# Kernel optimization log

Hardware: AMD Instinct MI355X
Metric: run time of the kernel (lower is better)

## Reference

```python
import jax, jax.numpy as jnp
import numpy as np


def setup_inputs() -> dict:
    key = jax.random.key(0)
    k1, k2, k3 = jax.random.split(key, 3)
    B, R, Din, D = 4096, 4096, 1024, 1024
    x = jax.random.normal(k1, (B, Din), dtype=jnp.float32)
    refs = jax.random.normal(k2, (R, Din), dtype=jnp.float32)
    W = jax.random.normal(k3, (Din, D), dtype=jnp.float32) * (1.0 / np.sqrt(Din))
    b = jnp.zeros((D,), dtype=jnp.float32)
    return {"x": x, "refs": refs, "W": W, "b": b}


def reference(x, refs, W, b) -> jnp.ndarray:
    # feature extractor (linear stand-in for the CResNet embedding)
    vin = x @ W + b          # (B, D)
    vrefs = refs @ W + b     # (R, D)
    # compute_degradation_metric: mean_r ||vin_b - vref_r||^2
    # = ||vin||^2 + mean_r ||vref_r||^2 - 2 * vin @ mean_r(vref_r)
    # Same math as the naive broadcast-sub-square-sum-mean, GEMM-friendly form.
    sq_in = jnp.sum(vin * vin, axis=1)                 # (B,)
    mean_sq_ref = jnp.mean(jnp.sum(vrefs * vrefs, axis=1))  # scalar
    mean_ref = jnp.mean(vrefs, axis=0)                 # (D,)
    cross = vin @ mean_ref                             # (B,)
    degradation_metric = sq_in + mean_sq_ref - 2.0 * cross
    return degradation_metric
```

## Files before the change

### kernel.cpp

```cpp
#include <hip/hip_runtime.h>
#include <hip/hip_bf16.h>
#include <stdint.h>


typedef __attribute__((ext_vector_type(8))) short short8;
typedef __attribute__((ext_vector_type(4))) float f32x4;

__device__ __forceinline__ short f2bf(float f) {
  uint32_t u = __builtin_bit_cast(uint32_t, f);
  uint32_t r = (u + 0x7fffu + ((u >> 16) & 1u)) >> 16;
  return (short)r;
}

#define WS_WT 0u
#define WS_TC 2097152u
#define WS_RR 2101248u

__global__ __launch_bounds__(256) void k_prep(
    const float* __restrict__ W, short* __restrict__ wt,
    float* __restrict__ tcol, float* __restrict__ refrow, float* __restrict__ out) {
  __shared__ short tile[64][68];
  const int b = blockIdx.x, t = threadIdx.x;
  if (b < 256) {
    const int tk = (b >> 4) * 64, tn = (b & 15) * 64;
    const int kk = t >> 4, nn4 = (t & 15) * 4;
#pragma unroll
    for (int p = 0; p < 4; ++p) {
      int k = kk + p * 16;
      float4 v = *(const float4*)&W[(size_t)(tk + k) * 1024 + tn + nn4];
      tile[nn4 + 0][k] = f2bf(v.x);
      tile[nn4 + 1][k] = f2bf(v.y);
      tile[nn4 + 2][k] = f2bf(v.z);
      tile[nn4 + 3][k] = f2bf(v.w);
    }
    __syncthreads();
    const int nn = t >> 4, kk4 = (t & 15) * 4;
#pragma unroll
    for (int p = 0; p < 4; ++p) {
      int n = nn + p * 16;
      uint32_t lo = (uint16_t)tile[n][kk4 + 0] | ((uint32_t)(uint16_t)tile[n][kk4 + 1] << 16);
      uint32_t hi = (uint16_t)tile[n][kk4 + 2] | ((uint32_t)(uint16_t)tile[n][kk4 + 3] << 16);
      *(uint2*)&wt[(size_t)(tn + n) * 1024 + tk + kk4] = make_uint2(lo, hi);
    }
  } else {
    const int i = (b - 256) * 256 + t;
    const float4 z = make_float4(0.f, 0.f, 0.f, 0.f);
    ((float4*)out)[i] = z;
    ((float4*)refrow)[i] = z;
    if (i < 256) ((float4*)tcol)[i] = z;
  }
}

template <bool IS_X>
__global__ __launch_bounds__(512, 4) void k_gemm(
    const float* __restrict__ Am, const short* __restrict__ Wt,
    const float* __restrict__ bias, float* __restrict__ tcol,
    float* __restrict__ refrow, float* __restrict__ out) {
  __shared__ __align__(16) short As[2][128 * 64];
  __shared__ __align__(16) short Bs[2][128 * 64];
  const int t = threadIdx.x;
  const int w = t >> 6, l = t & 63;

  if (IS_X && blockIdx.x >= 256) {
    __shared__ float sh[8];
    float s = 0.f;
    for (int i = t; i < 4096; i += 512) s += refrow[i];
#pragma unroll
    for (int off = 32; off; off >>= 1) s += __shfl_down(s, off, 64);
    if (l == 0) sh[w] = s;
    __syncthreads();
    if (t == 0) {
      float tot = 0.f;
#pragma unroll
      for (int i = 0; i < 8; ++i) tot += sh[i];
      sh[0] = tot * (1.0f / 4096.0f);
    }
    __syncthreads();
    const float ms = sh[0];
    for (int i = t; i < 4096; i += 512) atomicAdd(&out[i], ms);
    return;
  }

  const int wr = w >> 2, wc = w & 3;
  const int bx = blockIdx.x;
  const int mt = bx & 31;
  const int nt = bx >> 5;
  const int m0 = mt * 128;
  const int n0 = nt * 128;

  const int srow = t >> 3;
  const int sslot = t & 7;
  const int arow = t >> 4;
  const int acol = (t & 15) * 4;
  const int asl = (t & 15) >> 1, ah = t & 1;

  f32x4 acc[4][2] = {};
  float4 areg[4];

  auto stageB = [&](int buf, int kt) {
    const int k0 = kt * 64;
#pragma unroll
    for (int issue = 0; issue < 2; ++issue) {
      const int row = srow + issue * 64;
      const int sg = sslot ^ (row & 7);
      const short* gb = Wt + ((size_t)(n0 + row) * 1024 + k0 + sg * 8);
      char* lb = (char*)&Bs[buf][0] + issue * 8192 + w * 1024;
      __builtin_amdgcn_global_load_lds(
          (const __attribute__((address_space(1))) unsigned int*)gb,
          (__attribute__((address_space(3))) unsigned int*)lb, 16, 0, 0);
    }
  };
  auto loadA = [&](int kt) {
    const int k0 = kt * 64;
#pragma unroll
    for (int i = 0; i < 4; ++i) {
      const int r = arow + i * 32;
      areg[i] = *(const float4*)&Am[(size_t)(m0 + r) * 1024 + k0 + acol];
    }
  };
  auto writeA = [&](int buf) {
#pragma unroll
    for (int i = 0; i < 4; ++i) {
      const int r = arow + i * 32;
      uint32_t lo, hi;
      asm("v_cvt_pk_bf16_f32 %0, %1, %2" : "=v"(lo) : "v"(areg[i].x), "v"(areg[i].y));
      asm("v_cvt_pk_bf16_f32 %0, %1, %2" : "=v"(hi) : "v"(areg[i].z), "v"(areg[i].w));
      char* p = (char*)&As[buf][0] + r * 128 + (((asl ^ (r & 7)) * 16) + ah * 8);
      *(uint2*)p = make_uint2(lo, hi);
    }
  };

  loadA(0);
  stageB(0, 0);
  stageB(1, 1);
  writeA(0);
  loadA(1);

  for (int kt = 0; kt < 16; ++kt) {
    if (kt < 15) asm volatile("s_waitcnt vmcnt(6) lgkmcnt(0)" ::: "memory");
    else         asm volatile("s_waitcnt vmcnt(0) lgkmcnt(0)" ::: "memory");
    __builtin_amdgcn_s_barrier();
    const int cur = kt & 1;
    if (kt + 1 < 16) writeA((kt + 1) & 1);
    if (kt + 2 < 16) loadA(kt + 2);
#pragma unroll
    for (int kk = 0; kk < 2; ++kk) {
      short8 af[4], bfr[2];
#pragma unroll
      for (int i = 0; i < 4; ++i) {
        const int ra = wr * 64 + i * 16 + (l & 15);
        const int s = (l >> 4) + kk * 4;
        af[i] = *(const short8*)&As[cur][ra * 64 + ((s ^ (ra & 7)) * 8)];
      }
#pragma unroll
      for (int j = 0; j < 2; ++j) {
        const int rbw = wc * 32 + j * 16 + (l & 15);
        const int s = (l >> 4) + kk * 4;
        bfr[j] = *(const short8*)&Bs[cur][rbw * 64 + ((s ^ (rbw & 7)) * 8)];
      }
      __builtin_amdgcn_s_setprio(1);
#pragma unroll
      for (int i = 0; i < 4; ++i)
#pragma unroll
        for (int j = 0; j < 2; ++j)
          acc[i][j] = __builtin_amdgcn_mfma_f32_16x16x32_bf16(af[i], bfr[j], acc[i][j], 0, 0, 0);
      __builtin_amdgcn_s_setprio(0);
    }
    __builtin_amdgcn_s_barrier();
    if (kt + 2 < 16) stageB(cur, kt + 2);
  }

  float bv[2];
#pragma unroll
  for (int n2 = 0; n2 < 2; ++n2) bv[n2] = bias[n0 + wc * 32 + n2 * 16 + (l & 15)];

  if (IS_X) {
    float tvv[2];
#pragma unroll
    for (int n2 = 0; n2 < 2; ++n2)
      tvv[n2] = tcol[n0 + wc * 32 + n2 * 16 + (l & 15)] * (1.0f / 4096.0f);
#pragma unroll
    for (int m4 = 0; m4 < 4; ++m4) {
#pragma unroll
      for (int j = 0; j < 4; ++j) {
        float sq = 0.f, cr = 0.f;
#pragma unroll
        for (int n2 = 0; n2 < 2; ++n2) {
          const float v = acc[m4][n2][j] + bv[n2];
          sq += v * v;
          cr += v * tvv[n2];
        }
        float comb = sq - 2.0f * cr;
#pragma unroll
        for (int off = 1; off < 16; off <<= 1) comb += __shfl_xor(comb, off, 64);
        if ((l & 15) == 0) {
          const int rm = m0 + wr * 64 + m4 * 16 + (l >> 4) * 4 + j;
          atomicAdd(&out[rm], comb);
        }
      }
    }
  } else {
#pragma unroll
    for (int m4 = 0; m4 < 4; ++m4) {
#pragma unroll
      for (int j = 0; j < 4; ++j) {
        float sq = 0.f;
#pragma unroll
        for (int n2 = 0; n2 < 2; ++n2) {
          const float v = acc[m4][n2][j] + bv[n2];
          sq += v * v;
        }
#pragma unroll
        for (int off = 1; off < 16; off <<= 1) sq += __shfl_xor(sq, off, 64);
        if ((l & 15) == 0) {
          const int rm = m0 + wr * 64 + m4 * 16 + (l >> 4) * 4 + j;
          atomicAdd(&refrow[rm], sq);
        }
      }
    }
#pragma unroll
    for (int n2 = 0; n2 < 2; ++n2) {
      float cs = 16.0f * bv[n2];
#pragma unroll
      for (int m4 = 0; m4 < 4; ++m4)
#pragma unroll
        for (int j = 0; j < 4; ++j) cs += acc[m4][n2][j];
      cs += __shfl_xor(cs, 16, 64);
      cs += __shfl_xor(cs, 32, 64);
      if ((l >> 4) == 0)
        atomicAdd(&tcol[n0 + wc * 32 + n2 * 16 + (l & 15)], cs);
    }
  }
}

extern "C" void kernel_launch(void* const* d_in, const int* in_sizes, int n_in,
                              void* d_out, int out_size, void* d_ws, size_t ws_size,
                              hipStream_t stream) {
  const float* x    = (const float*)d_in[0];
  const float* refs = (const float*)d_in[1];
  const float* W    = (const float*)d_in[2];
  const float* bias = (const float*)d_in[3];
  float* out = (float*)d_out;
  char* ws = (char*)d_ws;

  short* wt     = (short*)(ws + WS_WT);
  float* tcol   = (float*)(ws + WS_TC);
  float* refrow = (float*)(ws + WS_RR);

  hipLaunchKernelGGL(k_prep, dim3(260), dim3(256), 0, stream, W, wt, tcol, refrow, out);
  hipLaunchKernelGGL(k_gemm<false>, dim3(256), dim3(512), 0, stream,
                     refs, wt, bias, tcol, refrow, out);
  hipLaunchKernelGGL(k_gemm<true>, dim3(257), dim3(512), 0, stream,
                     x, wt, bias, tcol, refrow, out);
}
```

Baseline: 51.54 us.

## Merge ref and x GEMMs into one launch with an atomic-counter dependency

Fuses the two GEMM launches into a single 512-block grid. The first 256 blocks process refs and bump a global counter. The x blocks run their GEMM mainloop, then spin until all ref blocks have finished before applying the mean-ref cross term. The final mean-square reduction moves into block 256. This removes a kernel-launch boundary and lets the x GEMM overlap the ref GEMM, but it relies on all blocks being co-resident (or ref blocks being scheduled first) to avoid deadlock.

```diff
diff --git a/kernel.cpp b/kernel.cpp
--- a/kernel.cpp
+++ b/kernel.cpp
@@ -15,10 +15,12 @@
 #define WS_WT 0u
 #define WS_TC 2097152u
 #define WS_RR 2101248u
+#define WS_CT 2117632u
 
 __global__ __launch_bounds__(256) void k_prep(
     const float* __restrict__ W, short* __restrict__ wt,
-    float* __restrict__ tcol, float* __restrict__ refrow, float* __restrict__ out) {
+    float* __restrict__ tcol, float* __restrict__ refrow,
+    unsigned int* __restrict__ ctr, float* __restrict__ out) {
   __shared__ short tile[64][68];
   const int b = blockIdx.x, t = threadIdx.x;
   if (b < 256) {
@@ -48,43 +50,27 @@
     ((float4*)out)[i] = z;
     ((float4*)refrow)[i] = z;
     if (i < 256) ((float4*)tcol)[i] = z;
+    if (b == 256 && t == 0) *ctr = 0u;
   }
 }
 
-template <bool IS_X>
 __global__ __launch_bounds__(512, 4) void k_gemm(
-    const float* __restrict__ Am, const short* __restrict__ Wt,
-    const float* __restrict__ bias, float* __restrict__ tcol,
-    float* __restrict__ refrow, float* __restrict__ out) {
+    const float* __restrict__ X, const float* __restrict__ R,
+    const short* __restrict__ Wt, const float* __restrict__ bias,
+    float* __restrict__ tcol, float* __restrict__ refrow,
+    unsigned int* __restrict__ ctr, float* __restrict__ out) {
   __shared__ __align__(16) short As[2][128 * 64];
   __shared__ __align__(16) short Bs[2][128 * 64];
+  __shared__ float redbuf[8];
   const int t = threadIdx.x;
   const int w = t >> 6, l = t & 63;
-
-  if (IS_X && blockIdx.x >= 256) {
-    __shared__ float sh[8];
-    float s = 0.f;
-    for (int i = t; i < 4096; i += 512) s += refrow[i];
-#pragma unroll
-    for (int off = 32; off; off >>= 1) s += __shfl_down(s, off, 64);
-    if (l == 0) sh[w] = s;
-    __syncthreads();
-    if (t == 0) {
-      float tot = 0.f;
-#pragma unroll
-      for (int i = 0; i < 8; ++i) tot += sh[i];
-      sh[0] = tot * (1.0f / 4096.0f);
-    }
-    __syncthreads();
-    const float ms = sh[0];
-    for (int i = t; i < 4096; i += 512) atomicAdd(&out[i], ms);
-    return;
-  }
-
   const int wr = w >> 2, wc = w & 3;
   const int bx = blockIdx.x;
-  const int mt = bx & 31;
-  const int nt = bx >> 5;
+  const bool is_ref = (bx < 256);
+  const int bh = bx & 255;
+  const int mt = bh & 31;
+  const int nt = (bh >> 5) & 7;
+  const float* Am = is_ref ? R : X;
   const int m0 = mt * 128;
   const int n0 = nt * 128;
 
@@ -174,32 +160,7 @@
 #pragma unroll
   for (int n2 = 0; n2 < 2; ++n2) bv[n2] = bias[n0 + wc * 32 + n2 * 16 + (l & 15)];
 
-  if (IS_X) {
-    float tvv[2];
-#pragma unroll
-    for (int n2 = 0; n2 < 2; ++n2)
-      tvv[n2] = tcol[n0 + wc * 32 + n2 * 16 + (l & 15)] * (1.0f / 4096.0f);
-#pragma unroll
-    for (int m4 = 0; m4 < 4; ++m4) {
-#pragma unroll
-      for (int j = 0; j < 4; ++j) {
-        float sq = 0.f, cr = 0.f;
-#pragma unroll
-        for (int n2 = 0; n2 < 2; ++n2) {
-          const float v = acc[m4][n2][j] + bv[n2];
-          sq += v * v;
-          cr += v * tvv[n2];
-        }
-        float comb = sq - 2.0f * cr;
-#pragma unroll
-        for (int off = 1; off < 16; off <<= 1) comb += __shfl_xor(comb, off, 64);
-        if ((l & 15) == 0) {
-          const int rm = m0 + wr * 64 + m4 * 16 + (l >> 4) * 4 + j;
-          atomicAdd(&out[rm], comb);
-        }
-      }
-    }
-  } else {
+  if (is_ref) {
 #pragma unroll
     for (int m4 = 0; m4 < 4; ++m4) {
 #pragma unroll
@@ -229,6 +190,59 @@
       cs += __shfl_xor(cs, 32, 64);
       if ((l >> 4) == 0)
         atomicAdd(&tcol[n0 + wc * 32 + n2 * 16 + (l & 15)], cs);
+    }
+    __syncthreads();
+    if (t == 0)
+      __hip_atomic_fetch_add(ctr, 1u, __ATOMIC_RELEASE, __HIP_MEMORY_SCOPE_AGENT);
+  } else {
+    if (t == 0) {
+      while (__hip_atomic_load(ctr, __ATOMIC_ACQUIRE, __HIP_MEMORY_SCOPE_AGENT) < 256u)
+        __builtin_amdgcn_s_sleep(8);
+    }
+    __syncthreads();
+    float tvv[2];
+#pragma unroll
+    for (int n2 = 0; n2 < 2; ++n2)
+      tvv[n2] = __hip_atomic_load(&tcol[n0 + wc * 32 + n2 * 16 + (l & 15)],
+                                  __ATOMIC_RELAXED, __HIP_MEMORY_SCOPE_AGENT) *
+                (1.0f / 4096.0f);
+#pragma unroll
+    for (int m4 = 0; m4 < 4; ++m4) {
+#pragma unroll
+      for (int j = 0; j < 4; ++j) {
+        float sq = 0.f, cr = 0.f;
+#pragma unroll
+        for (int n2 = 0; n2 < 2; ++n2) {
+          const float v = acc[m4][n2][j] + bv[n2];
+          sq += v * v;
+          cr += v * tvv[n2];
+        }
+        float comb = sq - 2.0f * cr;
+#pragma unroll
+        for (int off = 1; off < 16; off <<= 1) comb += __shfl_xor(comb, off, 64);
+        if ((l & 15) == 0) {
+          const int rm = m0 + wr * 64 + m4 * 16 + (l >> 4) * 4 + j;
+          atomicAdd(&out[rm], comb);
+        }
+      }
+    }
+    if (bx == 256) {
+      float s = 0.f;
+      for (int i = t; i < 4096; i += 512)
+        s += __hip_atomic_load(&refrow[i], __ATOMIC_RELAXED, __HIP_MEMORY_SCOPE_AGENT);
+#pragma unroll
+      for (int off = 32; off; off >>= 1) s += __shfl_down(s, off, 64);
+      if (l == 0) redbuf[w] = s;
+      __syncthreads();
+      if (t == 0) {
+        float tot = 0.f;
+#pragma unroll
+        for (int i = 0; i < 8; ++i) tot += redbuf[i];
+        redbuf[0] = tot * (1.0f / 4096.0f);
+      }
+      __syncthreads();
+      const float ms = redbuf[0];
+      for (int i = t; i < 4096; i += 512) atomicAdd(&out[i], ms);
     }
   }
 }
@@ -246,10 +260,9 @@
   short* wt     = (short*)(ws + WS_WT);
   float* tcol   = (float*)(ws + WS_TC);
   float* refrow = (float*)(ws + WS_RR);
-
-  hipLaunchKernelGGL(k_prep, dim3(260), dim3(256), 0, stream, W, wt, tcol, refrow, out);
-  hipLaunchKernelGGL(k_gemm<false>, dim3(256), dim3(512), 0, stream,
-                     refs, wt, bias, tcol, refrow, out);
-  hipLaunchKernelGGL(k_gemm<true>, dim3(257), dim3(512), 0, stream,
-                     x, wt, bias, tcol, refrow, out);
-}
+  unsigned int* ctr = (unsigned int*)(ws + WS_CT);
+
+  hipLaunchKernelGGL(k_prep, dim3(260), dim3(256), 0, stream, W, wt, tcol, refrow, ctr, out);
+  hipLaunchKernelGGL(k_gemm, dim3(512), dim3(512), 0, stream,
+                     x, refs, wt, bias, tcol, refrow, ctr, out);
+}
```

After: 60.75 us. 17.9% more time.
